# Performance work log

Measured on AMD Instinct MI355X. Metric: run time of the kernel, lower is better.

## Reference

```python
import jax, jax.numpy as jnp
import numpy as np

N_NODES = 50000
N_EDGES = 640000
M_DIM = 128
D_DIM = 128
H_DIM = M_DIM // 2
NORM_EPS = 1e-5


def setup_inputs() -> dict:
    key = jax.random.key(0)
    ks = jax.random.split(key, 8)
    messages = jax.random.normal(ks[0], (N_EDGES, M_DIM), dtype=jnp.float32)
    target_indices = jax.random.randint(ks[1], (N_EDGES,), 0, N_NODES, dtype=jnp.int64)
    node_features = jax.random.normal(ks[2], (N_NODES, D_DIM), dtype=jnp.float32)
    # attention scorer params (torch Linear: weight [out,in])
    W1 = 0.02 * jax.random.normal(ks[3], (H_DIM, M_DIM + D_DIM), dtype=jnp.float32)
    b1 = jnp.zeros((H_DIM,), dtype=jnp.float32)
    W2 = 0.02 * jax.random.normal(ks[4], (1, H_DIM), dtype=jnp.float32)
    gamma = jnp.ones((M_DIM,), dtype=jnp.float32)
    beta = jnp.zeros((M_DIM,), dtype=jnp.float32)
    return {"messages": messages, "target_indices": target_indices,
            "node_features": node_features, "n_nodes": N_NODES,
            "W1": W1, "b1": b1, "W2": W2, "gamma": gamma, "beta": beta}


def reference(messages, target_indices, node_features, n_nodes, W1, b1, W2, gamma, beta):
    # gather target node feats per edge: [E, D]
    target_feats = node_features[target_indices]
    attn_input = jnp.concatenate([messages, target_feats], axis=-1)  # [E, M+D]
    h = jax.nn.gelu(attn_input @ W1.T + b1, approximate=False)       # [E, M//2]
    raw_scores = (h @ W2.T)[:, 0]                                    # [E]
    weights = jax.nn.sigmoid(raw_scores)                             # [E]
    weighted = messages * weights[:, None]                           # [E, M]
    aggregated = jax.ops.segment_sum(weighted, target_indices, num_segments=n_nodes)  # [N, M]
    sum_weights = jax.ops.segment_sum(weights, target_indices, num_segments=n_nodes)  # [N]
    aggregated = aggregated / (sum_weights[:, None] + 1e-8)
    # LayerNorm over last dim
    mu = jnp.mean(aggregated, axis=-1, keepdims=True)
    var = jnp.var(aggregated, axis=-1, keepdims=True)
    normed = (aggregated - mu) * jax.lax.rsqrt(var + NORM_EPS)
    return normed * gamma + beta
```

## Files before the change

kernel.cpp:

```cpp
#include <hip/hip_runtime.h>
#include <hip/hip_bf16.h>

#define EDGES   640000
#define NNODES  50000
#define MDIM    128
#define HDIM    64
#define XSTR    36

typedef __attribute__((ext_vector_type(8))) short bshort8;
typedef __attribute__((ext_vector_type(4))) float f32x4;

__device__ __forceinline__ short f2bf(float f) {
    __hip_bfloat16 h = __float2bfloat16(f);
    return *reinterpret_cast<short*>(&h);
}

__global__ void k0_prep(const float* __restrict__ w1,
                        short* __restrict__ bpack, float* __restrict__ w1dt) {
    const int i = blockIdx.x * 256 + threadIdx.x;
    if (i < 8192) {
        const int ii   = i & 7;
        const int lane = (i >> 3) & 63;
        const int jtkc = i >> 9;
        const int kc = jtkc >> 2, jt = jtkc & 3;
        const int j = jt * 16 + (lane & 15);
        const int k = kc * 32 + (lane >> 4) * 8 + ii;
        bpack[i] = f2bf(w1[j * 256 + k]);
    } else if (i < 16384) {
        const int t = i - 8192;
        const int k = t >> 6, j = t & 63;
        w1dt[t] = w1[j * 256 + 128 + k];
    }
}

__global__ __launch_bounds__(256, 4) void kg_nodes(
    const float* __restrict__ feats, const float* __restrict__ w1dt,
    const float* __restrict__ b1, float* __restrict__ g)
{
    __shared__ float xs[4][64 * XSTR];
    const int wv = threadIdx.x >> 6, L = threadIdx.x & 63;
    const long base = ((long)blockIdx.x * 4 + wv) * 64;
    float* xb = xs[wv];
    float h[HDIM];
#pragma unroll
    for (int j = 0; j < HDIM; ++j) h[j] = 0.0f;
    const int gq = L >> 3, sub = L & 7;
    for (int c = 0; c < 4; ++c) {
        const int col0 = c * 32;
#pragma unroll
        for (int r = 0; r < 8; ++r) {
            long row = base + gq + 8 * r;
            if (row > NNODES - 1) row = NNODES - 1;
            float4 v = *(const float4*)(feats + row * MDIM + col0 + sub * 4);
            *(float4*)(xb + (gq + 8 * r) * XSTR + sub * 4) = v;
        }
        __syncthreads();
        for (int k4 = 0; k4 < 8; ++k4) {
            const float4 xv = *(const float4*)(xb + L * XSTR + 4 * k4);
            const float* colw = w1dt + (c * 32 + 4 * k4) * HDIM;
            const float xa[4] = {xv.x, xv.y, xv.z, xv.w};
#pragma unroll
            for (int kk = 0; kk < 4; ++kk) {
                const float xk = xa[kk];
#pragma unroll
                for (int j = 0; j < HDIM; ++j)
                    h[j] = fmaf(colw[kk * HDIM + j], xk, h[j]);
            }
        }
        __syncthreads();
    }
    const long row = base + L;
    if (row < NNODES) {
        float* gp = g + row * HDIM;
#pragma unroll
        for (int j4 = 0; j4 < 16; ++j4) {
            float4 b4 = *(const float4*)(b1 + 4 * j4);
            float4 o;
            o.x = h[4 * j4 + 0] + b4.x; o.y = h[4 * j4 + 1] + b4.y;
            o.z = h[4 * j4 + 2] + b4.z; o.w = h[4 * j4 + 3] + b4.w;
            *(float4*)(gp + 4 * j4) = o;
        }
    }
}

__global__ __launch_bounds__(256, 2) void k1_weights(
    const float* __restrict__ msgs, const int* __restrict__ tgt,
    const short* __restrict__ bpack, const float* __restrict__ g,
    const float* __restrict__ w2, float* __restrict__ weights,
    int* __restrict__ counts)
{
    __shared__ short lds[4][16 * 136];
    const int wv = threadIdx.x >> 6, L = threadIdx.x & 63;
    const long base = ((long)blockIdx.x * 4 + wv) * 16;
    short* xb = lds[wv];

    const bshort8* bp = (const bshort8*)bpack;
    bshort8 bfrag[16];
#pragma unroll
    for (int i = 0; i < 16; ++i) bfrag[i] = bp[i * 64 + L];

    const int se = L >> 5, k4 = L & 31;
#pragma unroll
    for (int r = 0; r < 8; ++r) {
        const int edge = 2 * r + se;
        const float4 v = *(const float4*)(msgs + (base + edge) * MDIM + k4 * 4);
        short4 s;
        s.x = f2bf(v.x); s.y = f2bf(v.y); s.z = f2bf(v.z); s.w = f2bf(v.w);
        *(short4*)(xb + edge * 136 + k4 * 4) = s;
    }
    __syncthreads();

    const int n = L & 15, quad = L >> 4;
    f32x4 acc[4];
#pragma unroll
    for (int jt = 0; jt < 4; ++jt) acc[jt] = (f32x4){0.f, 0.f, 0.f, 0.f};

#pragma unroll
    for (int kc = 0; kc < 4; ++kc) {
        const bshort8 a = *(const bshort8*)(xb + n * 136 + kc * 32 + quad * 8);
#pragma unroll
        for (int jt = 0; jt < 4; ++jt)
            acc[jt] = __builtin_amdgcn_mfma_f32_16x16x32_bf16(a, bfrag[kc * 4 + jt], acc[jt], 0, 0, 0);
    }

    float w2v[4];
#pragma unroll
    for (int jt = 0; jt < 4; ++jt) w2v[jt] = w2[jt * 16 + n];

#pragma unroll
    for (int r = 0; r < 4; ++r) {
        const long e = base + quad * 4 + r;
        const int t = tgt[e];
        const float* gp = g + (long)t * HDIM;
        float raw = 0.0f;
#pragma unroll
        for (int jt = 0; jt < 4; ++jt) {
            const float hj = acc[jt][r] + gp[jt * 16 + n];
            const float ge = 0.5f * hj * (1.0f + erff(hj * 0.70710678118654752f));
            raw = fmaf(ge, w2v[jt], raw);
        }
#pragma unroll
        for (int off = 1; off < 16; off <<= 1)
            raw += __shfl_xor(raw, off, 64);
        if (n == r) {
            weights[e] = 1.0f / (1.0f + __expf(-raw));
            atomicAdd(&counts[t], 1);
        }
    }
}

__global__ void kscan_local(const int* __restrict__ counts, int* __restrict__ offsets,
                            int* __restrict__ blocksums) {
    __shared__ int s[256];
    const int tid = threadIdx.x;
    const int i = blockIdx.x * 256 + tid;
    int v = (i < NNODES) ? counts[i] : 0;
    s[tid] = v;
    __syncthreads();
    for (int d = 1; d < 256; d <<= 1) {
        int t = (tid >= d) ? s[tid - d] : 0;
        __syncthreads();
        s[tid] += t;
        __syncthreads();
    }
    if (i < NNODES) offsets[i] = s[tid];
    if (tid == 255) blocksums[blockIdx.x] = s[255];
}

__global__ void kscan_blk(int* __restrict__ blocksums, int nblk) {
    __shared__ int s[256];
    const int tid = threadIdx.x;
    int v = (tid < nblk) ? blocksums[tid] : 0;
    s[tid] = v;
    __syncthreads();
    for (int d = 1; d < 256; d <<= 1) {
        int t = (tid >= d) ? s[tid - d] : 0;
        __syncthreads();
        s[tid] += t;
        __syncthreads();
    }
    if (tid < nblk) blocksums[tid] = s[tid] - v;
}

__global__ void kscan_fix(int* __restrict__ offsets, const int* __restrict__ blocksums,
                          const int* __restrict__ counts, int* __restrict__ cursor) {
    const int i = blockIdx.x * 256 + threadIdx.x;
    if (i < NNODES) {
        const int incl = offsets[i] + blocksums[i >> 8];
        offsets[i] = incl;
        cursor[i] = incl - counts[i];
    }
}

__global__ void kscatter(const int* __restrict__ tgt, int* __restrict__ cursor,
                         int* __restrict__ eidx) {
    const int e = blockIdx.x * 256 + threadIdx.x;
    if (e < EDGES) {
        const int pos = atomicAdd(&cursor[tgt[e]], 1);
        eidx[pos] = e;
    }
}

__global__ __launch_bounds__(256) void kagg(
    const float* __restrict__ msgs, const float* __restrict__ wts,
    const int* __restrict__ eidx, const int* __restrict__ offsets,
    const float* __restrict__ gamma, const float* __restrict__ beta,
    float* __restrict__ out)
{
    const int L = threadIdx.x & 63, wv = threadIdx.x >> 6;
    const int node = blockIdx.x * 4 + wv;
    if (node >= NNODES) return;
    const int end = offsets[node];
    const int beg = (node == 0) ? 0 : offsets[node - 1];
    float2 acc = {0.0f, 0.0f};
    float swl = 0.0f;
    for (int b = beg; b < end; b += 64) {
        int m = end - b; if (m > 64) m = 64;
        int eid = 0; float w = 0.0f;
        if (L < m) { eid = eidx[b + L]; w = wts[eid]; }
        swl += w;
        for (int i = 0; i < m; ++i) {
            const int e2 = __shfl(eid, i, 64);
            const float wi = __shfl(w, i, 64);
            const float2 mv = *(const float2*)(msgs + (long)e2 * MDIM + 2 * L);
            acc.x = fmaf(mv.x, wi, acc.x);
            acc.y = fmaf(mv.y, wi, acc.y);
        }
    }
    float s1 = acc.x + acc.y;
    float s2 = acc.x * acc.x + acc.y * acc.y;
#pragma unroll
    for (int off = 32; off; off >>= 1) {
        s1 += __shfl_xor(s1, off, 64);
        s2 += __shfl_xor(s2, off, 64);
        swl += __shfl_xor(swl, off, 64);
    }
    const float inv = 1.0f / (swl + 1e-8f);
    float2 a;
    a.x = acc.x * inv; a.y = acc.y * inv;
    const float mu = s1 * inv * (1.0f / MDIM);
    const float var = s2 * inv * inv * (1.0f / MDIM) - mu * mu;
    const float rs = rsqrtf(var + 1e-5f);
    const float2 gm = *(const float2*)(gamma + 2 * L);
    const float2 bt = *(const float2*)(beta + 2 * L);
    float2 o;
    o.x = (a.x - mu) * rs * gm.x + bt.x;
    o.y = (a.y - mu) * rs * gm.y + bt.y;
    *(float2*)(out + (long)node * MDIM + 2 * L) = o;
}

extern "C" void kernel_launch(void* const* d_in, const int* in_sizes, int n_in,
                              void* d_out, int out_size, void* d_ws, size_t ws_size,
                              hipStream_t stream) {
    const float* msgs  = (const float*)d_in[0];
    const int*   tgt   = (const int*)d_in[1];
    const float* feats = (const float*)d_in[2];
    const float* W1    = (const float*)d_in[4];
    const float* b1    = (const float*)d_in[5];
    const float* W2    = (const float*)d_in[6];
    const float* gamma = (const float*)d_in[7];
    const float* beta  = (const float*)d_in[8];
    float* out = (float*)d_out;

    char* ws = (char*)d_ws;
    short* bpack   = (short*)(ws + 0);
    float* w1dt    = (float*)(ws + (32 << 10));
    int*   counts  = (int*)  (ws + (64 << 10));
    int*   offsets = (int*)  (ws + (320 << 10));
    int*   cursor  = (int*)  (ws + (576 << 10));
    int*   bsums   = (int*)  (ws + (832 << 10));
    float* wts     = (float*)(ws + (1 << 20));
    int*   eidx    = (int*)  (ws + (4 << 20));
    float* g       = (float*)(ws + (8 << 20));

    hipMemsetAsync(counts, 0, NNODES * sizeof(int), stream);

    k0_prep<<<64, 256, 0, stream>>>(W1, bpack, w1dt);
    kg_nodes<<<(NNODES + 255) / 256, 256, 0, stream>>>(feats, w1dt, b1, g);
    k1_weights<<<EDGES / 64, 256, 0, stream>>>(msgs, tgt, bpack, g, W2, wts, counts);
    const int nblk = (NNODES + 255) / 256;
    kscan_local<<<nblk, 256, 0, stream>>>(counts, offsets, bsums);
    kscan_blk<<<1, 256, 0, stream>>>(bsums, nblk);
    kscan_fix<<<nblk, 256, 0, stream>>>(offsets, bsums, counts, cursor);
    kscatter<<<(EDGES + 255) / 256, 256, 0, stream>>>(tgt, cursor, eidx);
    kagg<<<(NNODES + 3) / 4, 256, 0, stream>>>(msgs, wts, eidx, offsets, gamma, beta, out);
}
```

Measured before the change: 675.2 us.

## Fuse edge attention scoring into CSR aggregation kernel, reading messages once

Removes the separate per-edge weight kernel and computes attention scores inside the per-node aggregation kernel. Each wave gathers 16 edge message rows at a time into LDS, runs bf16 MFMA for the hidden layer, and reuses the node's precomputed g row since every edge in the segment shares that target. The staged rows are then reused for the weighted sum, so messages are read from HBM once instead of twice. A separate histogram kernel now produces the counts, and erf is replaced by a polynomial approximation. The cost is padded MFMA work for nodes with few edges and worse load balance across nodes.

```diff
diff --git a/kernel.cpp b/kernel.cpp
--- a/kernel.cpp
+++ b/kernel.cpp
@@ -13,6 +13,21 @@
 __device__ __forceinline__ short f2bf(float f) {
     __hip_bfloat16 h = __float2bfloat16(f);
     return *reinterpret_cast<short*>(&h);
+}
+
+__device__ __forceinline__ float gelu_fast(float h) {
+    const float x  = h * 0.70710678118654752f;
+    const float ax = fabsf(x);
+    const float t  = __builtin_amdgcn_rcpf(fmaf(0.3275911f, ax, 1.0f));
+    float p = fmaf(1.061405429f, t, -1.453152027f);
+    p = fmaf(p, t,  1.421413741f);
+    p = fmaf(p, t, -0.284496736f);
+    p = fmaf(p, t,  0.254829592f);
+    p *= t;
+    const float e = __expf(-x * x);
+    float er = fmaf(-p, e, 1.0f);
+    er = (x < 0.0f) ? -er : er;
+    return 0.5f * h * (1.0f + er);
 }
 
 __global__ void k0_prep(const float* __restrict__ w1,
@@ -33,6 +48,11 @@
     }
 }
 
+__global__ void khist(const int* __restrict__ tgt, int* __restrict__ counts) {
+    const int e = blockIdx.x * 256 + threadIdx.x;
+    if (e < EDGES) atomicAdd(&counts[tgt[e]], 1);
+}
+
 __global__ __launch_bounds__(256, 4) void kg_nodes(
     const float* __restrict__ feats, const float* __restrict__ w1dt,
     const float* __restrict__ b1, float* __restrict__ g)
@@ -79,72 +99,6 @@
             o.x = h[4 * j4 + 0] + b4.x; o.y = h[4 * j4 + 1] + b4.y;
             o.z = h[4 * j4 + 2] + b4.z; o.w = h[4 * j4 + 3] + b4.w;
             *(float4*)(gp + 4 * j4) = o;
-        }
-    }
-}
-
-__global__ __launch_bounds__(256, 2) void k1_weights(
-    const float* __restrict__ msgs, const int* __restrict__ tgt,
-    const short* __restrict__ bpack, const float* __restrict__ g,
-    const float* __restrict__ w2, float* __restrict__ weights,
-    int* __restrict__ counts)
-{
-    __shared__ short lds[4][16 * 136];
-    const int wv = threadIdx.x >> 6, L = threadIdx.x & 63;
-    const long base = ((long)blockIdx.x * 4 + wv) * 16;
-    short* xb = lds[wv];
-
-    const bshort8* bp = (const bshort8*)bpack;
-    bshort8 bfrag[16];
-#pragma unroll
-    for (int i = 0; i < 16; ++i) bfrag[i] = bp[i * 64 + L];
-
-    const int se = L >> 5, k4 = L & 31;
-#pragma unroll
-    for (int r = 0; r < 8; ++r) {
-        const int edge = 2 * r + se;
-        const float4 v = *(const float4*)(msgs + (base + edge) * MDIM + k4 * 4);
-        short4 s;
-        s.x = f2bf(v.x); s.y = f2bf(v.y); s.z = f2bf(v.z); s.w = f2bf(v.w);
-        *(short4*)(xb + edge * 136 + k4 * 4) = s;
-    }
-    __syncthreads();
-
-    const int n = L & 15, quad = L >> 4;
-    f32x4 acc[4];
-#pragma unroll
-    for (int jt = 0; jt < 4; ++jt) acc[jt] = (f32x4){0.f, 0.f, 0.f, 0.f};
-
-#pragma unroll
-    for (int kc = 0; kc < 4; ++kc) {
-        const bshort8 a = *(const bshort8*)(xb + n * 136 + kc * 32 + quad * 8);
-#pragma unroll
-        for (int jt = 0; jt < 4; ++jt)
-            acc[jt] = __builtin_amdgcn_mfma_f32_16x16x32_bf16(a, bfrag[kc * 4 + jt], acc[jt], 0, 0, 0);
-    }
-
-    float w2v[4];
-#pragma unroll
-    for (int jt = 0; jt < 4; ++jt) w2v[jt] = w2[jt * 16 + n];
-
-#pragma unroll
-    for (int r = 0; r < 4; ++r) {
-        const long e = base + quad * 4 + r;
-        const int t = tgt[e];
-        const float* gp = g + (long)t * HDIM;
-        float raw = 0.0f;
-#pragma unroll
-        for (int jt = 0; jt < 4; ++jt) {
-            const float hj = acc[jt][r] + gp[jt * 16 + n];
-            const float ge = 0.5f * hj * (1.0f + erff(hj * 0.70710678118654752f));
-            raw = fmaf(ge, w2v[jt], raw);
-        }
-#pragma unroll
-        for (int off = 1; off < 16; off <<= 1)
-            raw += __shfl_xor(raw, off, 64);
-        if (n == r) {
-            weights[e] = 1.0f / (1.0f + __expf(-raw));
-            atomicAdd(&counts[t], 1);
         }
     }
 }
@@ -201,39 +155,99 @@
     }
 }
 
-__global__ __launch_bounds__(256) void kagg(
-    const float* __restrict__ msgs, const float* __restrict__ wts,
-    const int* __restrict__ eidx, const int* __restrict__ offsets,
+__global__ __launch_bounds__(256, 4) void kfused(
+    const float* __restrict__ msgs, const int* __restrict__ eidx,
+    const int* __restrict__ offsets, const short* __restrict__ bpack,
+    const float* __restrict__ g, const float* __restrict__ w2,
     const float* __restrict__ gamma, const float* __restrict__ beta,
     float* __restrict__ out)
 {
-    const int L = threadIdx.x & 63, wv = threadIdx.x >> 6;
+    __shared__ float lds[4][16][132];
+    const int wv = threadIdx.x >> 6, L = threadIdx.x & 63;
     const int node = blockIdx.x * 4 + wv;
     if (node >= NNODES) return;
     const int end = offsets[node];
     const int beg = (node == 0) ? 0 : offsets[node - 1];
+    const int m = end - beg;
+
+    const int n = L & 15, quad = L >> 4;
+    float (*xb)[132] = lds[wv];
+    const bshort8* bp = (const bshort8*)bpack;
+
+    float w2v[4], gv[4];
+    const float* gp = g + (long)node * HDIM;
+#pragma unroll
+    for (int jt = 0; jt < 4; ++jt) {
+        w2v[jt] = w2[jt * 16 + n];
+        gv[jt]  = gp[jt * 16 + n];
+    }
+
     float2 acc = {0.0f, 0.0f};
     float swl = 0.0f;
-    for (int b = beg; b < end; b += 64) {
-        int m = end - b; if (m > 64) m = 64;
-        int eid = 0; float w = 0.0f;
-        if (L < m) { eid = eidx[b + L]; w = wts[eid]; }
-        swl += w;
-        for (int i = 0; i < m; ++i) {
-            const int e2 = __shfl(eid, i, 64);
-            const float wi = __shfl(w, i, 64);
-            const float2 mv = *(const float2*)(msgs + (long)e2 * MDIM + 2 * L);
+
+    for (int t0 = 0; t0 < m; t0 += 16) {
+        const int sn = t0 + n;
+        const int eid = eidx[beg + ((sn < m) ? sn : 0)];
+        const float* rp = msgs + (long)eid * MDIM;
+
+        float4 v[8];
+#pragma unroll
+        for (int kc = 0; kc < 4; ++kc) {
+            v[2 * kc]     = *(const float4*)(rp + kc * 32 + quad * 8);
+            v[2 * kc + 1] = *(const float4*)(rp + kc * 32 + quad * 8 + 4);
+        }
+#pragma unroll
+        for (int kc = 0; kc < 4; ++kc) {
+            *(float4*)(&xb[n][kc * 32 + quad * 8])     = v[2 * kc];
+            *(float4*)(&xb[n][kc * 32 + quad * 8 + 4]) = v[2 * kc + 1];
+        }
+
+        f32x4 hacc[4];
+#pragma unroll
+        for (int jt = 0; jt < 4; ++jt) hacc[jt] = (f32x4){0.f, 0.f, 0.f, 0.f};
+#pragma unroll
+        for (int kc = 0; kc < 4; ++kc) {
+            const float4 va = v[2 * kc], vb = v[2 * kc + 1];
+            bshort8 a;
+            a[0] = f2bf(va.x); a[1] = f2bf(va.y); a[2] = f2bf(va.z); a[3] = f2bf(va.w);
+            a[4] = f2bf(vb.x); a[5] = f2bf(vb.y); a[6] = f2bf(vb.z); a[7] = f2bf(vb.w);
+#pragma unroll
+            for (int jt = 0; jt < 4; ++jt)
+                hacc[jt] = __builtin_amdgcn_mfma_f32_16x16x32_bf16(a, bp[(kc * 4 + jt) * 64 + L], hacc[jt], 0, 0, 0);
+        }
+
+        float wq[4];
+#pragma unroll
+        for (int r = 0; r < 4; ++r) {
+            float raw = 0.0f;
+#pragma unroll
+            for (int jt = 0; jt < 4; ++jt) {
+                const float hj = hacc[jt][r] + gv[jt];
+                raw = fmaf(gelu_fast(hj), w2v[jt], raw);
+            }
+#pragma unroll
+            for (int off = 1; off < 16; off <<= 1)
+                raw += __shfl_xor(raw, off, 64);
+            const int slot = t0 + quad * 4 + r;
+            wq[r] = (slot < m) ? __builtin_amdgcn_rcpf(1.0f + __expf(-raw)) : 0.0f;
+        }
+
+#pragma unroll
+        for (int i = 0; i < 16; ++i) {
+            const float wi = __shfl(wq[i & 3], (i >> 2) << 4, 64);
+            swl += wi;
+            const float2 mv = *(const float2*)(&xb[i][2 * L]);
             acc.x = fmaf(mv.x, wi, acc.x);
             acc.y = fmaf(mv.y, wi, acc.y);
         }
     }
+
     float s1 = acc.x + acc.y;
     float s2 = acc.x * acc.x + acc.y * acc.y;
 #pragma unroll
     for (int off = 32; off; off >>= 1) {
         s1 += __shfl_xor(s1, off, 64);
         s2 += __shfl_xor(s2, off, 64);
-        swl += __shfl_xor(swl, off, 64);
     }
     const float inv = 1.0f / (swl + 1e-8f);
     float2 a;
@@ -269,19 +283,18 @@
     int*   offsets = (int*)  (ws + (320 << 10));
     int*   cursor  = (int*)  (ws + (576 << 10));
     int*   bsums   = (int*)  (ws + (832 << 10));
-    float* wts     = (float*)(ws + (1 << 20));
     int*   eidx    = (int*)  (ws + (4 << 20));
     float* g       = (float*)(ws + (8 << 20));
 
     hipMemsetAsync(counts, 0, NNODES * sizeof(int), stream);
 
     k0_prep<<<64, 256, 0, stream>>>(W1, bpack, w1dt);
+    khist<<<(EDGES + 255) / 256, 256, 0, stream>>>(tgt, counts);
     kg_nodes<<<(NNODES + 255) / 256, 256, 0, stream>>>(feats, w1dt, b1, g);
-    k1_weights<<<EDGES / 64, 256, 0, stream>>>(msgs, tgt, bpack, g, W2, wts, counts);
     const int nblk = (NNODES + 255) / 256;
     kscan_local<<<nblk, 256, 0, stream>>>(counts, offsets, bsums);
     kscan_blk<<<1, 256, 0, stream>>>(bsums, nblk);
     kscan_fix<<<nblk, 256, 0, stream>>>(offsets, bsums, counts, cursor);
     kscatter<<<(EDGES + 255) / 256, 256, 0, stream>>>(tgt, cursor, eidx);
-    kagg<<<(NNODES + 3) / 4, 256, 0, stream>>>(msgs, wts, eidx, offsets, gamma, beta, out);
-}
+    kfused<<<(NNODES + 3) / 4, 256, 0, stream>>>(msgs, eidx, offsets, bpack, g, W2, gamma, beta, out);
+}
```

After: 695.7 us. 1.03x slower.

## Load MFMA operands directly from global, use fast GELU, and process two edges per gather step

Applied to the files above, without the earlier changes.

k1_weights now loads message rows straight into registers in MFMA A-fragment layout, so the LDS staging buffer and barrier are gone. It reads B fragments from global inside the loop instead of preloading 16 fragments, and relaxes the launch bounds. The exact erff GELU is replaced by the Abramowitz-Stegun polynomial erf approximation with a hardware reciprocal, which adds a small approximation error. kagg splits each wave into two halves that gather two edges per iteration with float4 loads, then combines the halves with a cross-lane shuffle before the LayerNorm reduction.

```diff
diff --git a/kernel.cpp b/kernel.cpp
--- a/kernel.cpp
+++ b/kernel.cpp
@@ -13,6 +13,21 @@
 __device__ __forceinline__ short f2bf(float f) {
     __hip_bfloat16 h = __float2bfloat16(f);
     return *reinterpret_cast<short*>(&h);
+}
+
+__device__ __forceinline__ float gelu_fast(float h) {
+    const float x  = h * 0.70710678118654752f;
+    const float ax = fabsf(x);
+    const float t  = __builtin_amdgcn_rcpf(fmaf(0.3275911f, ax, 1.0f));
+    float p = fmaf(1.061405429f, t, -1.453152027f);
+    p = fmaf(p, t,  1.421413741f);
+    p = fmaf(p, t, -0.284496736f);
+    p = fmaf(p, t,  0.254829592f);
+    p *= t;
+    const float e = __expf(-x * x);
+    float er = fmaf(-p, e, 1.0f);
+    er = (x < 0.0f) ? -er : er;
+    return 0.5f * h * (1.0f + er);
 }
 
 __global__ void k0_prep(const float* __restrict__ w1,
@@ -83,49 +98,42 @@
     }
 }
 
-__global__ __launch_bounds__(256, 2) void k1_weights(
+__global__ __launch_bounds__(256) void k1_weights(
     const float* __restrict__ msgs, const int* __restrict__ tgt,
     const short* __restrict__ bpack, const float* __restrict__ g,
     const float* __restrict__ w2, float* __restrict__ weights,
     int* __restrict__ counts)
 {
-    __shared__ short lds[4][16 * 136];
     const int wv = threadIdx.x >> 6, L = threadIdx.x & 63;
     const long base = ((long)blockIdx.x * 4 + wv) * 16;
-    short* xb = lds[wv];
-
+    const int n = L & 15, quad = L >> 4;
     const bshort8* bp = (const bshort8*)bpack;
-    bshort8 bfrag[16];
-#pragma unroll
-    for (int i = 0; i < 16; ++i) bfrag[i] = bp[i * 64 + L];
-
-    const int se = L >> 5, k4 = L & 31;
-#pragma unroll
-    for (int r = 0; r < 8; ++r) {
-        const int edge = 2 * r + se;
-        const float4 v = *(const float4*)(msgs + (base + edge) * MDIM + k4 * 4);
-        short4 s;
-        s.x = f2bf(v.x); s.y = f2bf(v.y); s.z = f2bf(v.z); s.w = f2bf(v.w);
-        *(short4*)(xb + edge * 136 + k4 * 4) = s;
-    }
-    __syncthreads();
-
-    const int n = L & 15, quad = L >> 4;
-    f32x4 acc[4];
-#pragma unroll
-    for (int jt = 0; jt < 4; ++jt) acc[jt] = (f32x4){0.f, 0.f, 0.f, 0.f};
-
+
+    const float* rp = msgs + (base + n) * MDIM + quad * 8;
+    float4 v[8];
 #pragma unroll
     for (int kc = 0; kc < 4; ++kc) {
-        const bshort8 a = *(const bshort8*)(xb + n * 136 + kc * 32 + quad * 8);
+        v[2 * kc]     = *(const float4*)(rp + kc * 32);
+        v[2 * kc + 1] = *(const float4*)(rp + kc * 32 + 4);
+    }
+
+    float w2v[4];
+#pragma unroll
+    for (int jt = 0; jt < 4; ++jt) w2v[jt] = w2[jt * 16 + n];
+
+    f32x4 hacc[4];
+#pragma unroll
+    for (int jt = 0; jt < 4; ++jt) hacc[jt] = (f32x4){0.f, 0.f, 0.f, 0.f};
+#pragma unroll
+    for (int kc = 0; kc < 4; ++kc) {
+        const float4 va = v[2 * kc], vb = v[2 * kc + 1];
+        bshort8 a;
+        a[0] = f2bf(va.x); a[1] = f2bf(va.y); a[2] = f2bf(va.z); a[3] = f2bf(va.w);
+        a[4] = f2bf(vb.x); a[5] = f2bf(vb.y); a[6] = f2bf(vb.z); a[7] = f2bf(vb.w);
 #pragma unroll
         for (int jt = 0; jt < 4; ++jt)
-            acc[jt] = __builtin_amdgcn_mfma_f32_16x16x32_bf16(a, bfrag[kc * 4 + jt], acc[jt], 0, 0, 0);
-    }
-
-    float w2v[4];
-#pragma unroll
-    for (int jt = 0; jt < 4; ++jt) w2v[jt] = w2[jt * 16 + n];
+            hacc[jt] = __builtin_amdgcn_mfma_f32_16x16x32_bf16(a, bp[(kc * 4 + jt) * 64 + L], hacc[jt], 0, 0, 0);
+    }
 
 #pragma unroll
     for (int r = 0; r < 4; ++r) {
@@ -135,9 +143,8 @@
         float raw = 0.0f;
 #pragma unroll
         for (int jt = 0; jt < 4; ++jt) {
-            const float hj = acc[jt][r] + gp[jt * 16 + n];
-            const float ge = 0.5f * hj * (1.0f + erff(hj * 0.70710678118654752f));
-            raw = fmaf(ge, w2v[jt], raw);
+            const float hj = hacc[jt][r] + gp[jt * 16 + n];
+            raw = fmaf(gelu_fast(hj), w2v[jt], raw);
         }
 #pragma unroll
         for (int off = 1; off < 16; off <<= 1)
@@ -212,41 +219,64 @@
     if (node >= NNODES) return;
     const int end = offsets[node];
     const int beg = (node == 0) ? 0 : offsets[node - 1];
-    float2 acc = {0.0f, 0.0f};
+
+    const int c0 = 4 * (L & 31);
+    const int half = L >> 5;
+    float4 acc = {0.0f, 0.0f, 0.0f, 0.0f};
     float swl = 0.0f;
+
     for (int b = beg; b < end; b += 64) {
         int m = end - b; if (m > 64) m = 64;
         int eid = 0; float w = 0.0f;
         if (L < m) { eid = eidx[b + L]; w = wts[eid]; }
         swl += w;
-        for (int i = 0; i < m; ++i) {
-            const int e2 = __shfl(eid, i, 64);
-            const float wi = __shfl(w, i, 64);
-            const float2 mv = *(const float2*)(msgs + (long)e2 * MDIM + 2 * L);
-            acc.x = fmaf(mv.x, wi, acc.x);
-            acc.y = fmaf(mv.y, wi, acc.y);
-        }
-    }
-    float s1 = acc.x + acc.y;
-    float s2 = acc.x * acc.x + acc.y * acc.y;
-#pragma unroll
-    for (int off = 32; off; off >>= 1) {
+        const int nit = (m + 1) >> 1;
+        for (int i = 0; i < nit; ++i) {
+            const int   e0 = __shfl(eid, 2 * i, 64);
+            const int   e1 = __shfl(eid, 2 * i + 1, 64);
+            const float w0 = __shfl(w,   2 * i, 64);
+            const float w1 = __shfl(w,   2 * i + 1, 64);
+            const int   er = half ? e1 : e0;
+            const float wr = half ? w1 : w0;
+            const float4 mv = *(const float4*)(msgs + (long)er * MDIM + c0);
+            acc.x = fmaf(mv.x, wr, acc.x);
+            acc.y = fmaf(mv.y, wr, acc.y);
+            acc.z = fmaf(mv.z, wr, acc.z);
+            acc.w = fmaf(mv.w, wr, acc.w);
+        }
+    }
+
+    acc.x += __shfl_xor(acc.x, 32, 64);
+    acc.y += __shfl_xor(acc.y, 32, 64);
+    acc.z += __shfl_xor(acc.z, 32, 64);
+    acc.w += __shfl_xor(acc.w, 32, 64);
+
+    float s1 = acc.x + acc.y + acc.z + acc.w;
+    float s2 = acc.x * acc.x + acc.y * acc.y + acc.z * acc.z + acc.w * acc.w;
+#pragma unroll
+    for (int off = 16; off; off >>= 1) {
         s1 += __shfl_xor(s1, off, 64);
         s2 += __shfl_xor(s2, off, 64);
+    }
+#pragma unroll
+    for (int off = 32; off; off >>= 1)
         swl += __shfl_xor(swl, off, 64);
-    }
+
     const float inv = 1.0f / (swl + 1e-8f);
-    float2 a;
-    a.x = acc.x * inv; a.y = acc.y * inv;
     const float mu = s1 * inv * (1.0f / MDIM);
     const float var = s2 * inv * inv * (1.0f / MDIM) - mu * mu;
     const float rs = rsqrtf(var + 1e-5f);
-    const float2 gm = *(const float2*)(gamma + 2 * L);
-    const float2 bt = *(const float2*)(beta + 2 * L);
-    float2 o;
-    o.x = (a.x - mu) * rs * gm.x + bt.x;
-    o.y = (a.y - mu) * rs * gm.y + bt.y;
-    *(float2*)(out + (long)node * MDIM + 2 * L) = o;
+
+    if (half == 0) {
+        const float4 gm = *(const float4*)(gamma + c0);
+        const float4 bt = *(const float4*)(beta + c0);
+        float4 o;
+        o.x = (acc.x * inv - mu) * rs * gm.x + bt.x;
+        o.y = (acc.y * inv - mu) * rs * gm.y + bt.y;
+        o.z = (acc.z * inv - mu) * rs * gm.z + bt.z;
+        o.w = (acc.w * inv - mu) * rs * gm.w + bt.w;
+        *(float4*)(out + (long)node * MDIM + c0) = o;
+    }
 }
 
 extern "C" void kernel_launch(void* const* d_in, const int* in_sizes, int n_in,
```

Result: faster. 632.3 us (-6.3%).
